# Optimization experiments

Hardware: AMD Instinct MI355X
Metric: run time of the kernel (lower is better)

Reference implementation:

```python
import jax, jax.numpy as jnp
from jax import lax
import numpy as np

V, E = 50000, 300          # word vocab / embedding dim
CV, CE = 200, 30           # char vocab / char embed dim
NF = 50                    # conv filters per kernel size
KS = (2, 3, 4)
H = 512                    # lstm hidden per direction
T = 20                     # num tags
B, S, C = 32, 256, 16      # batch, seq len, max chars per word
PAD = 0


def setup_inputs() -> dict:
    key = jax.random.key(0)
    ks = jax.random.split(key, 24)
    pos = jnp.arange(S)
    lengths = jax.random.randint(ks[0], (B,), S // 2, S + 1)
    mask = pos[None, :] < lengths[:, None]
    x = jnp.where(mask, jax.random.randint(ks[1], (B, S), 1, V), 0).astype(jnp.int32)
    x_chars = jnp.where(mask[:, :, None], jax.random.randint(ks[2], (B, S, C), 1, CV), 0).astype(jnp.int32)
    tags = jnp.where(mask, jax.random.randint(ks[3], (B, S), 1, T), 0).astype(jnp.int32)
    n = lambda k, sh, s=0.1: s * jax.random.normal(k, sh, jnp.float32)
    IN0 = E + NF * len(KS)  # 450 = lstm layer-0 input size
    return dict(
        x=x, x_chars=x_chars, tags=tags,
        word_embed=n(ks[4], (V, E)).at[PAD].set(0.0),
        char_embed=n(ks[5], (CV, CE)).at[0].set(0.0),
        conv_w2=n(ks[6], (NF, CE, 2)), conv_b2=n(ks[7], (NF,)),
        conv_w3=n(ks[8], (NF, CE, 3)), conv_b3=n(ks[9], (NF,)),
        conv_w4=n(ks[10], (NF, CE, 4)), conv_b4=n(ks[11], (NF,)),
        l0_wih=n(ks[12], (2, 4 * H, IN0), 0.04), l0_whh=n(ks[13], (2, 4 * H, H), 0.04),
        l0_bih=n(ks[14], (2, 4 * H), 0.04), l0_bhh=jnp.zeros((2, 4 * H), jnp.float32),
        l1_wih=n(ks[15], (2, 4 * H, 2 * H), 0.03), l1_whh=n(ks[16], (2, 4 * H, H), 0.03),
        l1_bih=n(ks[17], (2, 4 * H), 0.03), l1_bhh=jnp.zeros((2, 4 * H), jnp.float32),
        hw_Hw=n(ks[18], (2 * H, 2 * H), 0.02), hw_Hb=jnp.zeros((2 * H,), jnp.float32),
        hw_Tw=n(ks[19], (2 * H, 2 * H), 0.02), hw_Tb=-jnp.ones((2 * H,), jnp.float32),
        fc_w=n(ks[20], (T, 2 * H), 0.05), fc_b=jnp.zeros((T,), jnp.float32),
        crf_start=n(ks[21], (T,)), crf_end=n(ks[22], (T,)), crf_trans=n(ks[23], (T, T)),
    )


def _char_cnn(x_chars, char_embed, convs):
    b, s, c = x_chars.shape
    emb = char_embed[x_chars.reshape(b * s, c)].transpose(0, 2, 1)  # (B*S, CE, C)
    pooled = []
    for w, bias in convs:
        o = lax.conv_general_dilated(emb, w, (1,), 'VALID', dimension_numbers=('NCH', 'OIH', 'NCH'))
        pooled.append(jnp.max(jax.nn.relu(o + bias[None, :, None]), axis=-1))  # (B*S, NF)
    return jnp.concatenate(pooled, -1).reshape(b, s, -1)


def _lstm_dir(xs, wih, whh, bih, bhh, reverse):
    # xs: (S, B, in). PyTorch gate order: i, f, g, o.
    b = xs.shape[1]
    h = whh.shape[-1]
    bias = bih + bhh

    def step(carry, xt):
        hp, cp = carry
        g = xt @ wih.T + hp @ whh.T + bias
        i, f, gg, o = jnp.split(g, 4, axis=-1)
        cn = jax.nn.sigmoid(f) * cp + jax.nn.sigmoid(i) * jnp.tanh(gg)
        hn = jax.nn.sigmoid(o) * jnp.tanh(cn)
        return (hn, cn), hn

    init = (jnp.zeros((b, h), xs.dtype), jnp.zeros((b, h), xs.dtype))
    _, hs = lax.scan(step, init, xs, reverse=reverse)
    return hs  # (S, B, H), time-aligned with xs


def _bilstm_layer(xs, wih, whh, bih, bhh):
    fwd = _lstm_dir(xs, wih[0], whh[0], bih[0], bhh[0], False)
    bwd = _lstm_dir(xs, wih[1], whh[1], bih[1], bhh[1], True)
    return jnp.concatenate([fwd, bwd], axis=-1)


def _forward(x, x_chars, tags, word_embed, char_embed,
             conv_w2, conv_b2, conv_w3, conv_b3, conv_w4, conv_b4,
             l0_wih, l0_whh, l0_bih, l0_bhh, l1_wih, l1_whh, l1_bih, l1_bhh,
             hw_Hw, hw_Hb, hw_Tw, hw_Tb, fc_w, fc_b,
             crf_start, crf_end, crf_trans):
    mask = x != PAD  # (B, S)
    # ----- encoder (dropout = identity in eval) -----
    w_emb = word_embed[x]                              # (B, S, E)
    c_emb = _char_cnn(x_chars, char_embed,
                      [(conv_w2, conv_b2), (conv_w3, conv_b3), (conv_w4, conv_b4)])
    combined = jnp.concatenate([w_emb, c_emb], -1)     # (B, S, E+150)
    xs = combined.transpose(1, 0, 2)                   # (S, B, in)
    xs = _bilstm_layer(xs, l0_wih, l0_whh, l0_bih, l0_bhh)
    xs = _bilstm_layer(xs, l1_wih, l1_whh, l1_bih, l1_bhh)
    out = xs.transpose(1, 0, 2)                        # (B, S, 2H)
    t_gate = jax.nn.sigmoid(out @ hw_Tw.T + hw_Tb)
    out = t_gate * jax.nn.relu(out @ hw_Hw.T + hw_Hb) + (1.0 - t_gate) * out
    logits = out @ fc_w.T + fc_b                       # (B, S, T)

    # ----- CRF negative log-likelihood (torchcrf, reduction='mean') -----
    b, s, t = logits.shape
    maskf = mask.astype(logits.dtype)
    em_scores = jnp.take_along_axis(logits, tags[..., None], axis=-1)[..., 0]  # (B, S)
    trans_scores = crf_trans[tags[:, :-1], tags[:, 1:]]                        # (B, S-1)
    score = crf_start[tags[:, 0]] + em_scores[:, 0]
    score = score + jnp.sum(maskf[:, 1:] * (trans_scores + em_scores[:, 1:]), axis=1)
    last_idx = jnp.sum(mask, axis=1) - 1
    last_tags = tags[jnp.arange(b), last_idx]
    score = score + crf_end[last_tags]

    def fwd_step(alpha, inp):
        em_t, m_t = inp  # (B, T), (B,)
        nxt = jax.nn.logsumexp(alpha[:, :, None] + crf_trans[None] + em_t[:, None, :], axis=1)
        return jnp.where(m_t[:, None], nxt, alpha), None

    alpha0 = crf_start[None, :] + logits[:, 0]
    alpha, _ = lax.scan(fwd_step, alpha0,
                        (logits[:, 1:].transpose(1, 0, 2), mask[:, 1:].T))
    log_z = jax.nn.logsumexp(alpha + crf_end[None, :], axis=1)
    crf_loss = -jnp.mean(score - log_z)

    # ----- aux CE loss (ignore_index = PAD) -----
    lp = jax.nn.log_softmax(logits.reshape(b * s, t), axis=-1)
    nll = -jnp.take_along_axis(lp, tags.reshape(b * s, 1), axis=-1)[:, 0]
    valid = (tags.reshape(b * s) != PAD).astype(logits.dtype)
    aux = jnp.sum(nll * valid) / jnp.sum(valid)

    return crf_loss + 0.1 * aux


def reference(x, x_chars, tags, word_embed, char_embed,
              conv_w2, conv_b2, conv_w3, conv_b3, conv_w4, conv_b4,
              l0_wih, l0_whh, l0_bih, l0_bhh, l1_wih, l1_whh, l1_bih, l1_bhh,
              hw_Hw, hw_Hb, hw_Tw, hw_Tb, fc_w, fc_b,
              crf_start, crf_end, crf_trans):
    return _forward(x, x_chars, tags, word_embed, char_embed,
                    conv_w2, conv_b2, conv_w3, conv_b3, conv_w4, conv_b4,
                    l0_wih, l0_whh, l0_bih, l0_bhh, l1_wih, l1_whh, l1_bih, l1_bhh,
                    hw_Hw, hw_Hb, hw_Tw, hw_Tb, fc_w, fc_b,
                    crf_start, crf_end, crf_trans)
```

## Files before the change

kernel.cpp:

```cpp
#include <hip/hip_runtime.h>
#include <math.h>

#define B_   32
#define S_   256
#define T_   20
#define H_   512
#define E_   300
#define C_   16
#define CE_  30
#define NF_  50
#define IN0_ 450
#define KP0_ 480
#define G4_  2048
#define NG_  4096

typedef __attribute__((ext_vector_type(8))) short bf16x8;
typedef __attribute__((ext_vector_type(4))) float f32x4;

__device__ __forceinline__ float sigm(float x) { return 1.f / (1.f + __expf(-x)); }
__device__ __forceinline__ float tanhfast(float x) {
  x = fminf(15.f, fmaxf(-15.f, x));
  float e = __expf(-2.f * x);
  return (1.f - e) / (1.f + e);
}
__device__ __forceinline__ unsigned short f2bf(float f) {
  unsigned int u = __float_as_uint(f);
  unsigned int r = (u + 0x7fffu + ((u >> 16) & 1u)) >> 16;
  return (unsigned short)r;
}
__device__ __forceinline__ float bf2f(unsigned int u) {
  return __uint_as_float(u << 16);
}

#define GLOAD_LDS(gp, lp)                                                    \
  __builtin_amdgcn_global_load_lds(                                          \
      (const __attribute__((address_space(1))) void*)(gp),                   \
      (__attribute__((address_space(3))) void*)(lp), 16, 0, 0)

__global__ __launch_bounds__(256) void embed_cnn(
    const int* __restrict__ x, const int* __restrict__ xc,
    const float* __restrict__ wemb, const float* __restrict__ cemb,
    const float* __restrict__ w2, const float* __restrict__ cb2,
    const float* __restrict__ w3, const float* __restrict__ cb3,
    const float* __restrict__ w4, const float* __restrict__ cb4,
    unsigned short* __restrict__ out) {
  int m = blockIdx.x;
  int t = m >> 5, b = m & 31;
  int tid = threadIdx.x;
  __shared__ float emb[C_][CE_];
  __shared__ float conv[2100];

  int wid = x[b * S_ + t];
  for (int e = tid; e < KP0_; e += 256) {
    if (e < E_) out[(size_t)m * KP0_ + e] = f2bf(wemb[(size_t)wid * E_ + e]);
    else if (e >= IN0_) out[(size_t)m * KP0_ + e] = 0;
  }

  for (int idx = tid; idx < C_ * CE_; idx += 256) {
    int c = idx / CE_, ce = idx % CE_;
    int cid = xc[(b * S_ + t) * C_ + c];
    emb[c][ce] = cemb[cid * CE_ + ce];
  }
  __syncthreads();

  for (int idx = tid; idx < 2100; idx += 256) {
    int kw, f, p;
    const float* w; const float* bb;
    int r = idx;
    if (r < 750)      { kw = 2; f = r / 15; p = r % 15; w = w2; bb = cb2; }
    else if (r < 1450){ r -= 750;  kw = 3; f = r / 14; p = r % 14; w = w3; bb = cb3; }
    else              { r -= 1450; kw = 4; f = r / 13; p = r % 13; w = w4; bb = cb4; }
    float acc = bb[f];
    for (int j = 0; j < kw; ++j)
      for (int ce = 0; ce < CE_; ++ce)
        acc = fmaf(emb[p + j][ce], w[(f * CE_ + ce) * kw + j], acc);
    conv[idx] = fmaxf(acc, 0.f);
  }
  __syncthreads();

  if (tid < 150) {
    int kk = tid / 50, f = tid % 50;
    int base, np;
    if (kk == 0)      { base = f * 15;        np = 15; }
    else if (kk == 1) { base = 750 + f * 14;  np = 14; }
    else              { base = 1450 + f * 13; np = 13; }
    float mx = 0.f;
    for (int p = 0; p < np; ++p) mx = fmaxf(mx, conv[base + p]);
    out[(size_t)m * KP0_ + E_ + kk * 50 + f] = f2bf(mx);
  }
}

__global__ __launch_bounds__(256) void castpad(
    const float* __restrict__ src, unsigned short* __restrict__ dst,
    int R, int K, int Kp) {
  int i = blockIdx.x * 256 + threadIdx.x;
  if (i < R * Kp) {
    int r = i / Kp, k = i - r * Kp;
    dst[i] = (k < K) ? f2bf(src[(size_t)r * K + k]) : (unsigned short)0;
  }
}

__global__ __launch_bounds__(256) void gemm_bf16(
    const unsigned short* __restrict__ A, const unsigned short* __restrict__ W,
    const float* __restrict__ bias1, const float* __restrict__ bias2,
    float* __restrict__ C, int M, int N, int Kp) {
  __shared__ unsigned short As[128][32];
  __shared__ unsigned short Bs[128][32];
  int bm = blockIdx.y * 128, bn = blockIdx.x * 128;
  int tid = threadIdx.x;
  int wave = tid >> 6, lane = tid & 63;
  int wm = (wave & 1) * 64, wn = (wave >> 1) * 64;
  int l15 = lane & 15, l4 = lane >> 4;

  int srow = lane >> 2;
  int scol = (lane & 3) * 8;
  const unsigned short* ga0 = A + (size_t)(bm + wave * 32 + srow) * Kp + scol;
  const unsigned short* ga1 = A + (size_t)(bm + wave * 32 + 16 + srow) * Kp + scol;
  const unsigned short* gb0 = W + (size_t)(bn + wave * 32 + srow) * Kp + scol;
  const unsigned short* gb1 = W + (size_t)(bn + wave * 32 + 16 + srow) * Kp + scol;

  f32x4 acc[4][4];
#pragma unroll
  for (int i = 0; i < 4; ++i)
#pragma unroll
    for (int j = 0; j < 4; ++j) acc[i][j] = (f32x4){0.f, 0.f, 0.f, 0.f};

  for (int k0 = 0; k0 < Kp; k0 += 32) {
    __syncthreads();
    GLOAD_LDS(ga0 + k0, &As[wave * 32][0]);
    GLOAD_LDS(ga1 + k0, &As[wave * 32 + 16][0]);
    GLOAD_LDS(gb0 + k0, &Bs[wave * 32][0]);
    GLOAD_LDS(gb1 + k0, &Bs[wave * 32 + 16][0]);
    __syncthreads();

    bf16x8 af[4], bfv[4];
#pragma unroll
    for (int i = 0; i < 4; ++i) af[i]  = *(const bf16x8*)&As[wm + i * 16 + l15][l4 * 8];
#pragma unroll
    for (int j = 0; j < 4; ++j) bfv[j] = *(const bf16x8*)&Bs[wn + j * 16 + l15][l4 * 8];
#pragma unroll
    for (int i = 0; i < 4; ++i)
#pragma unroll
      for (int j = 0; j < 4; ++j)
        acc[i][j] = __builtin_amdgcn_mfma_f32_16x16x32_bf16(af[i], bfv[j], acc[i][j], 0, 0, 0);
  }

#pragma unroll
  for (int j = 0; j < 4; ++j) {
    int gn = bn + wn + j * 16 + l15;
    float bsum = (bias1 ? bias1[gn] : 0.f) + (bias2 ? bias2[gn] : 0.f);
#pragma unroll
    for (int i = 0; i < 4; ++i) {
#pragma unroll
      for (int r = 0; r < 4; ++r) {
        int gm = bm + wm + i * 16 + l4 * 4 + r;
        C[(size_t)gm * N + gn] = acc[i][j][r] + bsum;
      }
    }
  }
}

__global__ __launch_bounds__(512, 2) void lstm_scan(
    const float* __restrict__ P,
    const float* __restrict__ whh,
    unsigned short* __restrict__ Hbf,
    unsigned int* __restrict__ hT,
    int* __restrict__ flags) {
  int wg  = blockIdx.x;
  int dir = wg >> 5;
  int hb  = wg & 31;
  int tid = threadIdx.x;
  int wave = tid >> 6;
  int lane = tid & 63;
  int g  = wave & 3;
  int nb = wave >> 2;
  int l15 = lane & 15;
  int l4  = lane >> 4;

  int grow = g * H_ + hb * 16 + l15;
  const float* wrow = whh + ((size_t)dir * G4_ + grow) * H_;
  bf16x8 afrag[16];
#pragma unroll
  for (int kk = 0; kk < 16; ++kk) {
    int k0 = kk * 32 + l4 * 8;
    float4 lo = *(const float4*)(wrow + k0);
    float4 hi = *(const float4*)(wrow + k0 + 4);
    bf16x8 a;
    a[0] = (short)f2bf(lo.x); a[1] = (short)f2bf(lo.y);
    a[2] = (short)f2bf(lo.z); a[3] = (short)f2bf(lo.w);
    a[4] = (short)f2bf(hi.x); a[5] = (short)f2bf(hi.y);
    a[6] = (short)f2bf(hi.z); a[7] = (short)f2bf(hi.w);
    afrag[kk] = a;
  }

  __shared__ float lds_g[4][16][32];
  __shared__ unsigned short hlds[32][520];
  int* dflags = flags + dir * 32;

  bool pw = tid < 256;
  int pb = tid & 31, pq = (tid >> 5) & 7;
  float c0 = 0.f, c1 = 0.f;
  float2 pfc[4], pfn[4];

  {
    int t0i = dir ? (S_ - 1) : 0;
    if (pw) {
      size_t pr = ((size_t)(t0i * B_ + pb)) * NG_ + (size_t)dir * G4_ + hb * 16 + 2 * pq;
#pragma unroll
      for (int gg = 0; gg < 4; ++gg) pfc[gg] = *(const float2*)(P + pr + gg * H_);
    }
  }

  int srow   = wave * 4 + (lane & 3);
  int schunk = lane >> 2;
  const unsigned short* slabBase = (const unsigned short*)hT + (size_t)dir * (32 * 512);

  for (int s = 0; s < S_; ++s) {
    int t = dir ? (S_ - 1 - s) : s;

    f32x4 acc = {0.f, 0.f, 0.f, 0.f};
    if (s > 0) {
      const unsigned short* src = slabBase + (size_t)((s + 1) & 1) * (2 * 32 * 512)
                                  + srow * 512 + schunk * 32;
      bf16x8 t0, t1, t2, t3;
      asm volatile("global_load_dwordx4 %0, %1, off sc0 sc1"           : "=v"(t0) : "v"(src) : "memory");
      asm volatile("global_load_dwordx4 %0, %1, off offset:16 sc0 sc1" : "=v"(t1) : "v"(src) : "memory");
      asm volatile("global_load_dwordx4 %0, %1, off offset:32 sc0 sc1" : "=v"(t2) : "v"(src) : "memory");
      asm volatile("global_load_dwordx4 %0, %1, off offset:48 sc0 sc1" : "=v"(t3) : "v"(src) : "memory");
      if (pw && s < S_ - 1) {
        int tn = dir ? (S_ - 2 - s) : (s + 1);
        size_t pr = ((size_t)(tn * B_ + pb)) * NG_ + (size_t)dir * G4_ + hb * 16 + 2 * pq;
#pragma unroll
        for (int gg = 0; gg < 4; ++gg) pfn[gg] = *(const float2*)(P + pr + gg * H_);
        asm volatile("s_waitcnt vmcnt(4)" ::: "memory");
      } else {
        asm volatile("s_waitcnt vmcnt(0)" ::: "memory");
      }
      __builtin_amdgcn_sched_barrier(0);
      *(bf16x8*)&hlds[srow][schunk * 32 +  0] = t0;
      *(bf16x8*)&hlds[srow][schunk * 32 +  8] = t1;
      *(bf16x8*)&hlds[srow][schunk * 32 + 16] = t2;
      *(bf16x8*)&hlds[srow][schunk * 32 + 24] = t3;
      __syncthreads();

      bf16x8 bv[16];
#pragma unroll
      for (int kk = 0; kk < 16; ++kk)
        bv[kk] = *(const bf16x8*)&hlds[nb * 16 + l15][kk * 32 + l4 * 8];
#pragma unroll
      for (int kk = 0; kk < 16; ++kk)
        acc = __builtin_amdgcn_mfma_f32_16x16x32_bf16(afrag[kk], bv[kk], acc, 0, 0, 0);
    } else {
      if (pw) {
        int tn = dir ? (S_ - 2) : 1;
        size_t pr = ((size_t)(tn * B_ + pb)) * NG_ + (size_t)dir * G4_ + hb * 16 + 2 * pq;
#pragma unroll
        for (int gg = 0; gg < 4; ++gg) pfn[gg] = *(const float2*)(P + pr + gg * H_);
      }
    }

#pragma unroll
    for (int r = 0; r < 4; ++r)
      lds_g[g][l4 * 4 + r][l15 + 16 * nb] = acc[r];
    __syncthreads();

    if (pw) {
      int h0 = 2 * pq, h1 = 2 * pq + 1;
      float iv0 = lds_g[0][h0][pb] + pfc[0].x, iv1 = lds_g[0][h1][pb] + pfc[0].y;
      float fv0 = lds_g[1][h0][pb] + pfc[1].x, fv1 = lds_g[1][h1][pb] + pfc[1].y;
      float gv0 = lds_g[2][h0][pb] + pfc[2].x, gv1 = lds_g[2][h1][pb] + pfc[2].y;
      float ov0 = lds_g[3][h0][pb] + pfc[3].x, ov1 = lds_g[3][h1][pb] + pfc[3].y;
      float cn0 = sigm(fv0) * c0 + sigm(iv0) * tanhfast(gv0);
      float cn1 = sigm(fv1) * c1 + sigm(iv1) * tanhfast(gv1);
      float hn0 = sigm(ov0) * tanhfast(cn0);
      float hn1 = sigm(ov1) * tanhfast(cn1);
      c0 = cn0; c1 = cn1;
      unsigned int hp = (unsigned int)f2bf(hn0) | ((unsigned int)f2bf(hn1) << 16);
      *(unsigned int*)(Hbf + ((size_t)(t * B_ + pb)) * 1024 + dir * H_ + hb * 16 + 2 * pq) = hp;
      unsigned int* hc = hT + ((((size_t)(s & 1) * 2 + dir) * 32 + pb) * 256 + hb * 8 + pq);
      __hip_atomic_store(hc, hp, __ATOMIC_RELAXED, __HIP_MEMORY_SCOPE_AGENT);
#pragma unroll
      for (int gg = 0; gg < 4; ++gg) pfc[gg] = pfn[gg];
    }

    if (s < S_ - 1) {
      __syncthreads();
      if (wave == 0) {
        int target = s + 1;
        if (lane == 0)
          __hip_atomic_store(dflags + hb, target, __ATOMIC_RELAXED, __HIP_MEMORY_SCOPE_AGENT);
        int guard = 0;
        for (;;) {
          int v = target;
          if (lane < 32)
            v = __hip_atomic_load(dflags + lane, __ATOMIC_RELAXED, __HIP_MEMORY_SCOPE_AGENT);
          if (__all(v >= target)) break;
          __builtin_amdgcn_s_sleep(1);
          if (++guard > (1 << 17)) break;
        }
      }
      __syncthreads();
    }
  }
}

__global__ __launch_bounds__(256) void hwfc_k(
    const unsigned int* __restrict__ Xbf,
    const float* __restrict__ G1,
    const float* __restrict__ G2,
    const float* __restrict__ fc_w,
    const float* __restrict__ fc_b,
    float* __restrict__ LOG) {
  int m = blockIdx.x;
  int tid = threadIdx.x;
  int wave = tid >> 6, lane = tid & 63;
  int e0 = tid * 4;

  unsigned int xv0 = Xbf[(size_t)m * 512 + tid * 2];
  unsigned int xv1 = Xbf[(size_t)m * 512 + tid * 2 + 1];
  float4 g1 = *(const float4*)(G1 + (size_t)m * 1024 + e0);
  float4 g2 = *(const float4*)(G2 + (size_t)m * 1024 + e0);
  float tg, o[4];
  tg = sigm(g1.x); o[0] = tg * fmaxf(g2.x, 0.f) + (1.f - tg) * bf2f(xv0 & 0xffffu);
  tg = sigm(g1.y); o[1] = tg * fmaxf(g2.y, 0.f) + (1.f - tg) * bf2f(xv0 >> 16);
  tg = sigm(g1.z); o[2] = tg * fmaxf(g2.z, 0.f) + (1.f - tg) * bf2f(xv1 & 0xffffu);
  tg = sigm(g1.w); o[3] = tg * fmaxf(g2.w, 0.f) + (1.f - tg) * bf2f(xv1 >> 16);

  float acc[T_];
#pragma unroll
  for (int j = 0; j < T_; ++j) {
    float4 w = *(const float4*)(fc_w + (size_t)j * 1024 + e0);
    acc[j] = o[0] * w.x + o[1] * w.y + o[2] * w.z + o[3] * w.w;
  }
#pragma unroll
  for (int off = 32; off > 0; off >>= 1)
#pragma unroll
    for (int j = 0; j < T_; ++j)
      acc[j] += __shfl_xor(acc[j], off);

  __shared__ float part[4][T_];
  if (lane == 0)
#pragma unroll
    for (int j = 0; j < T_; ++j) part[wave][j] = acc[j];
  __syncthreads();
  if (tid < T_)
    LOG[(size_t)m * T_ + tid] =
        part[0][tid] + part[1][tid] + part[2][tid] + part[3][tid] + fc_b[tid];
}

__global__ __launch_bounds__(256) void crf_score_k(
    const int* __restrict__ x, const int* __restrict__ tags,
    const float* __restrict__ L,
    const float* __restrict__ cstart, const float* __restrict__ cend,
    const float* __restrict__ ctrans, float* __restrict__ score) {
  int b = blockIdx.x;
  int t = threadIdx.x;
  int tg = tags[b * S_ + t];
  float part = 0.f;
  bool valid;
  if (t == 0) {
    part = cstart[tg] + L[(size_t)b * T_ + tg];
    valid = true;
  } else {
    valid = (x[b * S_ + t] != 0);
    if (valid)
      part = ctrans[tags[b * S_ + t - 1] * T_ + tg] + L[((size_t)t * B_ + b) * T_ + tg];
  }
  bool nextInvalid = (t == S_ - 1) || (x[b * S_ + t + 1] == 0);
  if (valid && nextInvalid) part += cend[tg];

  __shared__ float red[256];
  red[t] = part;
  __syncthreads();
  for (int off = 128; off > 0; off >>= 1) {
    if (t < off) red[t] += red[t + off];
    __syncthreads();
  }
  if (t == 0) score[b] = red[0];
}

__global__ __launch_bounds__(64) void crf_forward_k(
    const int* __restrict__ x, const float* __restrict__ L,
    const float* __restrict__ cstart, const float* __restrict__ cend,
    const float* __restrict__ ctrans, float* __restrict__ logz) {
  int b = blockIdx.x;
  int tp = threadIdx.x;
  __shared__ float alpha[T_];
  __shared__ float trT[T_][T_];
  for (int i = tp; i < T_ * T_; i += 64)
    trT[i / T_][i % T_] = ctrans[(i % T_) * T_ + (i / T_)];
  if (tp < T_) alpha[tp] = cstart[tp] + L[(size_t)b * T_ + tp];
  __syncthreads();
  for (int t = 1; t < S_; ++t) {
    float newv = 0.f;
    bool active = tp < T_;
    bool msk = x[b * S_ + t] != 0;
    if (active) {
      float em = L[((size_t)t * B_ + b) * T_ + tp];
      float mx = -1e30f;
#pragma unroll
      for (int tt = 0; tt < T_; ++tt) mx = fmaxf(mx, alpha[tt] + trT[tp][tt]);
      float sum = 0.f;
#pragma unroll
      for (int tt = 0; tt < T_; ++tt) sum += __expf(alpha[tt] + trT[tp][tt] - mx);
      float nxt = mx + __logf(sum) + em;
      newv = msk ? nxt : alpha[tp];
    }
    __syncthreads();
    if (active) alpha[tp] = newv;
    __syncthreads();
  }
  if (tp == 0) {
    float mx = -1e30f;
    for (int tt = 0; tt < T_; ++tt) mx = fmaxf(mx, alpha[tt] + cend[tt]);
    float sum = 0.f;
    for (int tt = 0; tt < T_; ++tt) sum += __expf(alpha[tt] + cend[tt] - mx);
    logz[b] = mx + __logf(sum);
  }
}

__global__ __launch_bounds__(256) void nll_k(const float* __restrict__ L,
                                             const int* __restrict__ tags,
                                             float* __restrict__ accum) {
  int m = blockIdx.x * 256 + threadIdx.x;
  float nv = 0.f, vv = 0.f;
  if (m < B_ * S_) {
    int t = m >> 5, b = m & 31;
    int tg = tags[b * S_ + t];
    const float* row = L + (size_t)m * T_;
    float mx = -1e30f;
    for (int i = 0; i < T_; ++i) mx = fmaxf(mx, row[i]);
    float sum = 0.f;
    for (int i = 0; i < T_; ++i) sum += expf(row[i] - mx);
    float lse = mx + logf(sum);
    if (tg != 0) { nv = lse - row[tg]; vv = 1.f; }
  }
  __shared__ float sn[256], sv[256];
  int tid = threadIdx.x;
  sn[tid] = nv; sv[tid] = vv;
  __syncthreads();
  for (int off = 128; off > 0; off >>= 1) {
    if (tid < off) { sn[tid] += sn[tid + off]; sv[tid] += sv[tid + off]; }
    __syncthreads();
  }
  if (tid == 0) { atomicAdd(&accum[0], sn[0]); atomicAdd(&accum[1], sv[0]); }
}

__global__ void final_k(const float* __restrict__ score, const float* __restrict__ logz,
                        const float* __restrict__ accum, float* __restrict__ out) {
  if (threadIdx.x == 0 && blockIdx.x == 0) {
    float s = 0.f;
    for (int b = 0; b < B_; ++b) s += score[b] - logz[b];
    float crf = -s / (float)B_;
    out[0] = crf + 0.1f * (accum[0] / accum[1]);
  }
}

extern "C" void kernel_launch(void* const* d_in, const int* in_sizes, int n_in,
                              void* d_out, int out_size, void* d_ws, size_t ws_size,
                              hipStream_t stream) {
  (void)in_sizes; (void)n_in; (void)out_size; (void)ws_size;
  const int*   x      = (const int*)d_in[0];
  const int*   xc     = (const int*)d_in[1];
  const int*   tags   = (const int*)d_in[2];
  const float* wemb   = (const float*)d_in[3];
  const float* cemb   = (const float*)d_in[4];
  const float* w2     = (const float*)d_in[5];
  const float* cb2    = (const float*)d_in[6];
  const float* w3     = (const float*)d_in[7];
  const float* cb3    = (const float*)d_in[8];
  const float* w4     = (const float*)d_in[9];
  const float* cb4    = (const float*)d_in[10];
  const float* l0_wih = (const float*)d_in[11];
  const float* l0_whh = (const float*)d_in[12];
  const float* l0_bih = (const float*)d_in[13];
  const float* l0_bhh = (const float*)d_in[14];
  const float* l1_wih = (const float*)d_in[15];
  const float* l1_whh = (const float*)d_in[16];
  const float* l1_bih = (const float*)d_in[17];
  const float* l1_bhh = (const float*)d_in[18];
  const float* hw_Hw  = (const float*)d_in[19];
  const float* hw_Hb  = (const float*)d_in[20];
  const float* hw_Tw  = (const float*)d_in[21];
  const float* hw_Tb  = (const float*)d_in[22];
  const float* fc_w   = (const float*)d_in[23];
  const float* fc_b   = (const float*)d_in[24];
  const float* cstart = (const float*)d_in[25];
  const float* cend   = (const float*)d_in[26];
  const float* ctrans = (const float*)d_in[27];

  float* ws    = (float*)d_ws;
  float* P     = ws;
  float* G1    = P;
  float* G2    = P + 8388608;
  unsigned short* Hbf    = (unsigned short*)(ws + 33554432);
  unsigned short* COMBbf = (unsigned short*)(ws + 37748736);
  unsigned short* Wbf    = (unsigned short*)(ws + 39714816);
  float* LOG   = ws + 41811968;
  unsigned int* hT = (unsigned int*)(ws + 41975808);
  int*   flags = (int*)(ws + 42008576);
  float* score = ws + 42008576 + 128;
  float* logz  = score + 32;
  float* accum = logz + 32;

  hipMemsetAsync(accum, 0, 2 * sizeof(float), stream);

  embed_cnn<<<B_ * S_, 256, 0, stream>>>(x, xc, wemb, cemb, w2, cb2, w3, cb3, w4, cb4, COMBbf);

  castpad<<<(4096 * KP0_ + 255) / 256, 256, 0, stream>>>(l0_wih, Wbf, 4096, IN0_, KP0_);
  {
    dim3 g(NG_ / 128, (B_ * S_) / 128);
    gemm_bf16<<<g, 256, 0, stream>>>(COMBbf, Wbf, l0_bih, l0_bhh, P, B_ * S_, NG_, KP0_);
  }
  hipMemsetAsync(flags, 0, 128 * sizeof(int), stream);
  lstm_scan<<<64, 512, 0, stream>>>(P, l0_whh, Hbf, hT, flags);

  castpad<<<(4096 * 1024 + 255) / 256, 256, 0, stream>>>(l1_wih, Wbf, 4096, 1024, 1024);
  {
    dim3 g(NG_ / 128, (B_ * S_) / 128);
    gemm_bf16<<<g, 256, 0, stream>>>(Hbf, Wbf, l1_bih, l1_bhh, P, B_ * S_, NG_, 1024);
  }
  hipMemsetAsync(flags, 0, 128 * sizeof(int), stream);
  lstm_scan<<<64, 512, 0, stream>>>(P, l1_whh, Hbf, hT, flags);

  {
    dim3 g(1024 / 128, (B_ * S_) / 128);
    castpad<<<(1024 * 1024 + 255) / 256, 256, 0, stream>>>(hw_Tw, Wbf, 1024, 1024, 1024);
    gemm_bf16<<<g, 256, 0, stream>>>(Hbf, Wbf, hw_Tb, nullptr, G1, B_ * S_, 1024, 1024);
    castpad<<<(1024 * 1024 + 255) / 256, 256, 0, stream>>>(hw_Hw, Wbf, 1024, 1024, 1024);
    gemm_bf16<<<g, 256, 0, stream>>>(Hbf, Wbf, hw_Hb, nullptr, G2, B_ * S_, 1024, 1024);
  }
  hwfc_k<<<B_ * S_, 256, 0, stream>>>(
      (const unsigned int*)Hbf, G1, G2, fc_w, fc_b, LOG);

  crf_score_k<<<B_, 256, 0, stream>>>(x, tags, LOG, cstart, cend, ctrans, score);
  crf_forward_k<<<B_, 64, 0, stream>>>(x, LOG, cstart, cend, ctrans, logz);
  nll_k<<<(B_ * S_ + 255) / 256, 256, 0, stream>>>(LOG, tags, accum);
  final_k<<<1, 64, 0, stream>>>(score, logz, accum, (float*)d_out);
}
```

Measured before the change: 3.362 ms.

## Halve LSTM scan workgroups and interleave gate rows to drop LDS gate exchange

The recurrent LSTM scan now runs on 32 workgroups instead of 64, each covering 32 hidden units. The W_hh rows are interleaved so that one MFMA output tile holds all four gates for a hidden unit. Each wave then computes two batch-half MFMA chains, and every lane applies the cell update directly from its accumulators. This removes the LDS gate buffer and one __syncthreads per timestep, and halves the number of workgroups taking part in the flag barrier. The cost is twice the MFMA work and P loads per workgroup, and a shuffle to pack the bf16 pairs before the stores.

```diff
diff --git a/kernel.cpp b/kernel.cpp
--- a/kernel.cpp
+++ b/kernel.cpp
@@ -160,25 +160,26 @@
   }
 }
 
-__global__ __launch_bounds__(512, 2) void lstm_scan(
+__global__ __launch_bounds__(512, 1) void lstm_scan(
     const float* __restrict__ P,
     const float* __restrict__ whh,
-    unsigned short* __restrict__ Hbf,
+    unsigned int* __restrict__ Hbf32,
     unsigned int* __restrict__ hT,
     int* __restrict__ flags) {
   int wg  = blockIdx.x;
-  int dir = wg >> 5;
-  int hb  = wg & 31;
+  int dir = wg >> 4;
+  int hb  = wg & 15;
+  int hbase = hb * 32;
   int tid = threadIdx.x;
   int wave = tid >> 6;
   int lane = tid & 63;
-  int g  = wave & 3;
-  int nb = wave >> 2;
   int l15 = lane & 15;
   int l4  = lane >> 4;
-
-  int grow = g * H_ + hb * 16 + l15;
-  const float* wrow = whh + ((size_t)dir * G4_ + grow) * H_;
+  int hidx = hbase + wave * 4 + l4;
+
+  int arow_h = hbase + wave * 4 + (l15 >> 2);
+  int arow_g = l15 & 3;
+  const float* wrow = whh + ((size_t)dir * G4_ + arow_g * H_ + arow_h) * H_;
   bf16x8 afrag[16];
 #pragma unroll
   for (int kk = 0; kk < 16; ++kk) {
@@ -193,21 +194,20 @@
     afrag[kk] = a;
   }
 
-  __shared__ float lds_g[4][16][32];
   __shared__ unsigned short hlds[32][520];
   int* dflags = flags + dir * 32;
 
-  bool pw = tid < 256;
-  int pb = tid & 31, pq = (tid >> 5) & 7;
   float c0 = 0.f, c1 = 0.f;
-  float2 pfc[4], pfn[4];
+  float pfc0[4], pfc1[4], pfn0[4], pfn1[4];
 
   {
     int t0i = dir ? (S_ - 1) : 0;
-    if (pw) {
-      size_t pr = ((size_t)(t0i * B_ + pb)) * NG_ + (size_t)dir * G4_ + hb * 16 + 2 * pq;
-#pragma unroll
-      for (int gg = 0; gg < 4; ++gg) pfc[gg] = *(const float2*)(P + pr + gg * H_);
+    size_t pr0 = ((size_t)(t0i * B_ + l15)) * NG_ + (size_t)dir * G4_ + hidx;
+    size_t pr1 = ((size_t)(t0i * B_ + 16 + l15)) * NG_ + (size_t)dir * G4_ + hidx;
+#pragma unroll
+    for (int gg = 0; gg < 4; ++gg) {
+      pfc0[gg] = P[pr0 + gg * H_];
+      pfc1[gg] = P[pr1 + gg * H_];
     }
   }
 
@@ -218,7 +218,8 @@
   for (int s = 0; s < S_; ++s) {
     int t = dir ? (S_ - 1 - s) : s;
 
-    f32x4 acc = {0.f, 0.f, 0.f, 0.f};
+    f32x4 acc0 = {0.f, 0.f, 0.f, 0.f};
+    f32x4 acc1 = {0.f, 0.f, 0.f, 0.f};
     if (s > 0) {
       const unsigned short* src = slabBase + (size_t)((s + 1) & 1) * (2 * 32 * 512)
                                   + srow * 512 + schunk * 32;
@@ -227,12 +228,16 @@
       asm volatile("global_load_dwordx4 %0, %1, off offset:16 sc0 sc1" : "=v"(t1) : "v"(src) : "memory");
       asm volatile("global_load_dwordx4 %0, %1, off offset:32 sc0 sc1" : "=v"(t2) : "v"(src) : "memory");
       asm volatile("global_load_dwordx4 %0, %1, off offset:48 sc0 sc1" : "=v"(t3) : "v"(src) : "memory");
-      if (pw && s < S_ - 1) {
+      if (s < S_ - 1) {
         int tn = dir ? (S_ - 2 - s) : (s + 1);
-        size_t pr = ((size_t)(tn * B_ + pb)) * NG_ + (size_t)dir * G4_ + hb * 16 + 2 * pq;
-#pragma unroll
-        for (int gg = 0; gg < 4; ++gg) pfn[gg] = *(const float2*)(P + pr + gg * H_);
-        asm volatile("s_waitcnt vmcnt(4)" ::: "memory");
+        size_t pr0 = ((size_t)(tn * B_ + l15)) * NG_ + (size_t)dir * G4_ + hidx;
+        size_t pr1 = ((size_t)(tn * B_ + 16 + l15)) * NG_ + (size_t)dir * G4_ + hidx;
+#pragma unroll
+        for (int gg = 0; gg < 4; ++gg) {
+          pfn0[gg] = P[pr0 + gg * H_];
+          pfn1[gg] = P[pr1 + gg * H_];
+        }
+        asm volatile("s_waitcnt vmcnt(8)" ::: "memory");
       } else {
         asm volatile("s_waitcnt vmcnt(0)" ::: "memory");
       }
@@ -243,44 +248,49 @@
       *(bf16x8*)&hlds[srow][schunk * 32 + 24] = t3;
       __syncthreads();
 
-      bf16x8 bv[16];
-#pragma unroll
-      for (int kk = 0; kk < 16; ++kk)
-        bv[kk] = *(const bf16x8*)&hlds[nb * 16 + l15][kk * 32 + l4 * 8];
-#pragma unroll
-      for (int kk = 0; kk < 16; ++kk)
-        acc = __builtin_amdgcn_mfma_f32_16x16x32_bf16(afrag[kk], bv[kk], acc, 0, 0, 0);
+#pragma unroll
+      for (int kk = 0; kk < 16; ++kk) {
+        bf16x8 b0 = *(const bf16x8*)&hlds[l15][kk * 32 + l4 * 8];
+        bf16x8 b1 = *(const bf16x8*)&hlds[16 + l15][kk * 32 + l4 * 8];
+        acc0 = __builtin_amdgcn_mfma_f32_16x16x32_bf16(afrag[kk], b0, acc0, 0, 0, 0);
+        acc1 = __builtin_amdgcn_mfma_f32_16x16x32_bf16(afrag[kk], b1, acc1, 0, 0, 0);
+      }
     } else {
-      if (pw) {
-        int tn = dir ? (S_ - 2) : 1;
-        size_t pr = ((size_t)(tn * B_ + pb)) * NG_ + (size_t)dir * G4_ + hb * 16 + 2 * pq;
-#pragma unroll
-        for (int gg = 0; gg < 4; ++gg) pfn[gg] = *(const float2*)(P + pr + gg * H_);
+      int tn = dir ? (S_ - 2) : 1;
+      size_t pr0 = ((size_t)(tn * B_ + l15)) * NG_ + (size_t)dir * G4_ + hidx;
+      size_t pr1 = ((size_t)(tn * B_ + 16 + l15)) * NG_ + (size_t)dir * G4_ + hidx;
+#pragma unroll
+      for (int gg = 0; gg < 4; ++gg) {
+        pfn0[gg] = P[pr0 + gg * H_];
+        pfn1[gg] = P[pr1 + gg * H_];
       }
     }
 
-#pragma unroll
-    for (int r = 0; r < 4; ++r)
-      lds_g[g][l4 * 4 + r][l15 + 16 * nb] = acc[r];
-    __syncthreads();
-
-    if (pw) {
-      int h0 = 2 * pq, h1 = 2 * pq + 1;
-      float iv0 = lds_g[0][h0][pb] + pfc[0].x, iv1 = lds_g[0][h1][pb] + pfc[0].y;
-      float fv0 = lds_g[1][h0][pb] + pfc[1].x, fv1 = lds_g[1][h1][pb] + pfc[1].y;
-      float gv0 = lds_g[2][h0][pb] + pfc[2].x, gv1 = lds_g[2][h1][pb] + pfc[2].y;
-      float ov0 = lds_g[3][h0][pb] + pfc[3].x, ov1 = lds_g[3][h1][pb] + pfc[3].y;
-      float cn0 = sigm(fv0) * c0 + sigm(iv0) * tanhfast(gv0);
-      float cn1 = sigm(fv1) * c1 + sigm(iv1) * tanhfast(gv1);
-      float hn0 = sigm(ov0) * tanhfast(cn0);
-      float hn1 = sigm(ov1) * tanhfast(cn1);
-      c0 = cn0; c1 = cn1;
-      unsigned int hp = (unsigned int)f2bf(hn0) | ((unsigned int)f2bf(hn1) << 16);
-      *(unsigned int*)(Hbf + ((size_t)(t * B_ + pb)) * 1024 + dir * H_ + hb * 16 + 2 * pq) = hp;
-      unsigned int* hc = hT + ((((size_t)(s & 1) * 2 + dir) * 32 + pb) * 256 + hb * 8 + pq);
-      __hip_atomic_store(hc, hp, __ATOMIC_RELAXED, __HIP_MEMORY_SCOPE_AGENT);
-#pragma unroll
-      for (int gg = 0; gg < 4; ++gg) pfc[gg] = pfn[gg];
+    {
+      float iv0 = acc0[0] + pfc0[0], fv0 = acc0[1] + pfc0[1];
+      float gv0 = acc0[2] + pfc0[2], ov0 = acc0[3] + pfc0[3];
+      float iv1 = acc1[0] + pfc1[0], fv1 = acc1[1] + pfc1[1];
+      float gv1 = acc1[2] + pfc1[2], ov1 = acc1[3] + pfc1[3];
+      c0 = sigm(fv0) * c0 + sigm(iv0) * tanhfast(gv0);
+      c1 = sigm(fv1) * c1 + sigm(iv1) * tanhfast(gv1);
+      float hn0 = sigm(ov0) * tanhfast(c0);
+      float hn1 = sigm(ov1) * tanhfast(c1);
+      unsigned int m0 = (unsigned int)f2bf(hn0);
+      unsigned int m1 = (unsigned int)f2bf(hn1);
+      unsigned int p0 = (unsigned int)__shfl_xor((int)m0, 16);
+      unsigned int p1 = (unsigned int)__shfl_xor((int)m1, 16);
+      if ((l4 & 1) == 0) {
+        unsigned int w0 = m0 | (p0 << 16);
+        unsigned int w1 = m1 | (p1 << 16);
+        int hw = hidx >> 1;
+        Hbf32[((size_t)(t * B_ + l15)) * 512 + dir * 256 + hw] = w0;
+        Hbf32[((size_t)(t * B_ + 16 + l15)) * 512 + dir * 256 + hw] = w1;
+        unsigned int* hc = hT + (((size_t)(s & 1) * 2 + dir) * 32) * 256;
+        __hip_atomic_store(hc + (size_t)l15 * 256 + hw,        w0, __ATOMIC_RELAXED, __HIP_MEMORY_SCOPE_AGENT);
+        __hip_atomic_store(hc + (size_t)(16 + l15) * 256 + hw, w1, __ATOMIC_RELAXED, __HIP_MEMORY_SCOPE_AGENT);
+      }
+#pragma unroll
+      for (int gg = 0; gg < 4; ++gg) { pfc0[gg] = pfn0[gg]; pfc1[gg] = pfn1[gg]; }
     }
 
     if (s < S_ - 1) {
@@ -292,7 +302,7 @@
         int guard = 0;
         for (;;) {
           int v = target;
-          if (lane < 32)
+          if (lane < 16)
             v = __hip_atomic_load(dflags + lane, __ATOMIC_RELAXED, __HIP_MEMORY_SCOPE_AGENT);
           if (__all(v >= target)) break;
           __builtin_amdgcn_s_sleep(1);
@@ -513,7 +523,7 @@
     gemm_bf16<<<g, 256, 0, stream>>>(COMBbf, Wbf, l0_bih, l0_bhh, P, B_ * S_, NG_, KP0_);
   }
   hipMemsetAsync(flags, 0, 128 * sizeof(int), stream);
-  lstm_scan<<<64, 512, 0, stream>>>(P, l0_whh, Hbf, hT, flags);
+  lstm_scan<<<32, 512, 0, stream>>>(P, l0_whh, (unsigned int*)Hbf, hT, flags);
 
   castpad<<<(4096 * 1024 + 255) / 256, 256, 0, stream>>>(l1_wih, Wbf, 4096, 1024, 1024);
   {
@@ -521,7 +531,7 @@
     gemm_bf16<<<g, 256, 0, stream>>>(Hbf, Wbf, l1_bih, l1_bhh, P, B_ * S_, NG_, 1024);
   }
   hipMemsetAsync(flags, 0, 128 * sizeof(int), stream);
-  lstm_scan<<<64, 512, 0, stream>>>(P, l1_whh, Hbf, hT, flags);
+  lstm_scan<<<32, 512, 0, stream>>>(P, l1_whh, (unsigned int*)Hbf, hT, flags);
 
   {
     dim3 g(1024 / 128, (B_ * S_) / 128);
```

Result: slower. 3.945 ms (+17.3%).
